# Kernel tuning notes

Measured on AMD Instinct MI355X. Metric: run time of the kernel, lower is better.

Reference implementation:

```python
import jax, jax.numpy as jnp
import numpy as np

B, F = 16384, 2048


def setup_inputs() -> dict:
    key = jax.random.key(0)
    k0, k1 = jax.random.split(key)
    x0 = jax.random.normal(k0, (B, F), dtype=jnp.float32)
    x = jax.random.normal(k1, (B, F), dtype=jnp.float32)
    # Parameters as initialized by the torch module
    weights = jnp.ones((F,), dtype=jnp.float32)
    bias = jnp.zeros((F,), dtype=jnp.float32)
    return {"x0": x0, "x": x, "weights": weights, "bias": bias}


def reference(x0, x, weights, bias):
    # torch: bmm(x0[:, :, None], x[:, None, :]) @ weights + bias + x
    # The [B,F,F] outer product contracted with weights over the last axis
    # equals x0 * (x . weights), computed in O(B*F) without the F^2 tensor.
    xw = jnp.einsum('bf,f->b', x, weights)  # [B]
    return x0 * xw[:, None] + bias + x
```

## Files before the change

### kernel.cpp

```cpp
#include <hip/hip_runtime.h>


#define F_DIM 2048

__global__ __launch_bounds__(256) void cross_row_kernel(
    const float* __restrict__ x0,
    const float* __restrict__ x,
    const float* __restrict__ w,
    const float* __restrict__ bias,
    float* __restrict__ out)
{
    const int b = blockIdx.x;
    const int t = threadIdx.x;
    const long long row = (long long)b * F_DIM;

    const float4* __restrict__ x4  = (const float4*)(x  + row);
    const float4* __restrict__ x04 = (const float4*)(x0 + row);
    const float4* __restrict__ w4  = (const float4*)w;
    const float4* __restrict__ bi4 = (const float4*)bias;
    float4* __restrict__ o4 = (float4*)(out + row);

    float4 xa = x4[t];
    float4 xb = x4[t + 256];
    float4 wa = w4[t];
    float4 wb = w4[t + 256];

    float4 x0a = x04[t];
    float4 x0b = x04[t + 256];
    float4 ba  = bi4[t];
    float4 bb  = bi4[t + 256];

    float partial = xa.x * wa.x + xa.y * wa.y + xa.z * wa.z + xa.w * wa.w
                  + xb.x * wb.x + xb.y * wb.y + xb.z * wb.z + xb.w * wb.w;

    #pragma unroll
    for (int off = 32; off > 0; off >>= 1)
        partial += __shfl_down(partial, off, 64);

    __shared__ float sdot[4];
    __shared__ float dot_s;
    const int wave = t >> 6;
    const int lane = t & 63;
    if (lane == 0) sdot[wave] = partial;
    __syncthreads();
    if (t == 0) dot_s = sdot[0] + sdot[1] + sdot[2] + sdot[3];
    __syncthreads();
    const float dot = dot_s;

    float4 oa, ob;
    oa.x = x0a.x * dot + ba.x + xa.x;
    oa.y = x0a.y * dot + ba.y + xa.y;
    oa.z = x0a.z * dot + ba.z + xa.z;
    oa.w = x0a.w * dot + ba.w + xa.w;
    ob.x = x0b.x * dot + bb.x + xb.x;
    ob.y = x0b.y * dot + bb.y + xb.y;
    ob.z = x0b.z * dot + bb.z + xb.z;
    ob.w = x0b.w * dot + bb.w + xb.w;

    o4[t]       = oa;
    o4[t + 256] = ob;
}

extern "C" void kernel_launch(void* const* d_in, const int* in_sizes, int n_in,
                              void* d_out, int out_size, void* d_ws, size_t ws_size,
                              hipStream_t stream) {
    const float* x0   = (const float*)d_in[0];
    const float* x    = (const float*)d_in[1];
    const float* w    = (const float*)d_in[2];
    const float* bias = (const float*)d_in[3];
    float* out = (float*)d_out;

    const int B = in_sizes[0] / F_DIM;
    cross_row_kernel<<<B, 256, 0, stream>>>(x0, x, w, bias, out);
}
```

Measured before the change: 304.5 us.

## Assign one row per wavefront to drop block-level reduction barriers

Each 64-lane wavefront now owns a whole row of 2048 floats, holding 8 float4 slots of x and x0 in registers. The block-wide shared-memory reduction and its two __syncthreads are replaced by an xor-shuffle reduction inside the wave, and the grid shrinks to B/4 blocks. This removes barrier stalls and gives more loads in flight per thread, at the cost of higher register use. The launch assumes B is divisible by 4.

```diff
diff --git a/kernel.cpp b/kernel.cpp
--- a/kernel.cpp
+++ b/kernel.cpp
@@ -2,6 +2,7 @@
 
 
 #define F_DIM 2048
+#define SLOTS 8
 
 __global__ __launch_bounds__(256) void cross_row_kernel(
     const float* __restrict__ x0,
@@ -10,55 +11,46 @@
     const float* __restrict__ bias,
     float* __restrict__ out)
 {
-    const int b = blockIdx.x;
-    const int t = threadIdx.x;
-    const long long row = (long long)b * F_DIM;
+    const int wave = threadIdx.x >> 6;
+    const int lane = threadIdx.x & 63;
+    const long long b = (long long)blockIdx.x * 4 + wave;
+    const long long row = b * (long long)F_DIM;
 
     const float4* __restrict__ x4  = (const float4*)(x  + row);
     const float4* __restrict__ x04 = (const float4*)(x0 + row);
     const float4* __restrict__ w4  = (const float4*)w;
     const float4* __restrict__ bi4 = (const float4*)bias;
-    float4* __restrict__ o4 = (float4*)(out + row);
+    float4*       __restrict__ o4  = (float4*)(out + row);
 
-    float4 xa = x4[t];
-    float4 xb = x4[t + 256];
-    float4 wa = w4[t];
-    float4 wb = w4[t + 256];
+    float4 xr[SLOTS], x0r[SLOTS];
+    #pragma unroll
+    for (int i = 0; i < SLOTS; ++i) xr[i]  = x4 [lane + 64 * i];
+    #pragma unroll
+    for (int i = 0; i < SLOTS; ++i) x0r[i] = x04[lane + 64 * i];
 
-    float4 x0a = x04[t];
-    float4 x0b = x04[t + 256];
-    float4 ba  = bi4[t];
-    float4 bb  = bi4[t + 256];
-
-    float partial = xa.x * wa.x + xa.y * wa.y + xa.z * wa.z + xa.w * wa.w
-                  + xb.x * wb.x + xb.y * wb.y + xb.z * wb.z + xb.w * wb.w;
+    float partial = 0.0f;
+    #pragma unroll
+    for (int i = 0; i < SLOTS; ++i) {
+        const float4 wv = w4[lane + 64 * i];
+        partial += xr[i].x * wv.x + xr[i].y * wv.y
+                 + xr[i].z * wv.z + xr[i].w * wv.w;
+    }
 
     #pragma unroll
     for (int off = 32; off > 0; off >>= 1)
-        partial += __shfl_down(partial, off, 64);
+        partial += __shfl_xor(partial, off, 64);
+    const float dot = partial;
 
-    __shared__ float sdot[4];
-    __shared__ float dot_s;
-    const int wave = t >> 6;
-    const int lane = t & 63;
-    if (lane == 0) sdot[wave] = partial;
-    __syncthreads();
-    if (t == 0) dot_s = sdot[0] + sdot[1] + sdot[2] + sdot[3];
-    __syncthreads();
-    const float dot = dot_s;
-
-    float4 oa, ob;
-    oa.x = x0a.x * dot + ba.x + xa.x;
-    oa.y = x0a.y * dot + ba.y + xa.y;
-    oa.z = x0a.z * dot + ba.z + xa.z;
-    oa.w = x0a.w * dot + ba.w + xa.w;
-    ob.x = x0b.x * dot + bb.x + xb.x;
-    ob.y = x0b.y * dot + bb.y + xb.y;
-    ob.z = x0b.z * dot + bb.z + xb.z;
-    ob.w = x0b.w * dot + bb.w + xb.w;
-
-    o4[t]       = oa;
-    o4[t + 256] = ob;
+    #pragma unroll
+    for (int i = 0; i < SLOTS; ++i) {
+        const float4 bv = bi4[lane + 64 * i];
+        float4 o;
+        o.x = x0r[i].x * dot + (bv.x + xr[i].x);
+        o.y = x0r[i].y * dot + (bv.y + xr[i].y);
+        o.z = x0r[i].z * dot + (bv.z + xr[i].z);
+        o.w = x0r[i].w * dot + (bv.w + xr[i].w);
+        o4[lane + 64 * i] = o;
+    }
 }
 
 extern "C" void kernel_launch(void* const* d_in, const int* in_sizes, int n_in,
@@ -71,5 +63,5 @@
     float* out = (float*)d_out;
 
     const int B = in_sizes[0] / F_DIM;
-    cross_row_kernel<<<B, 256, 0, stream>>>(x0, x, w, bias, out);
+    cross_row_kernel<<<B / 4, 256, 0, stream>>>(x0, x, w, bias, out);
 }
```

Result: slower. 311.3 us (+2.2%).
